# Optimization experiments

Measured on AMD Instinct MI355X. Metric: run time of the kernel, lower is better.

The kernel has to match this reference:

```python
import jax, jax.numpy as jnp
import numpy as np

B, S, D, H, C, E, V = 8, 2048, 1024, 512, 256, 64, 64


def setup_inputs() -> dict:
    key = jax.random.key(0)
    ks = jax.random.split(key, 40)
    ri = lambda i, hi: jax.random.randint(ks[i], (B, S), 0, hi).astype(jnp.int32)
    p = lambda i, shape: (jax.random.normal(ks[i], shape, jnp.float32) * 0.02)
    inp = {
        'h_x': jax.random.normal(ks[0], (B, S, D), jnp.float32),
        'h_y': jax.random.normal(ks[1], (B, S, D), jnp.float32),
        'x_mask': jnp.ones((B, S), jnp.int32),
        'y_mask': jnp.ones((B, S), jnp.int32),
        'src_token_dense_mask': ri(2, 2), 'src_token_sparse_mask': ri(3, 2),
        'src_token_inarc_type': ri(4, V), 'src_token_arc_head': ri(5, S),
        'src_token_depth': ri(6, 16), 'src_word_inarc_type': ri(7, V),
        'src_word_inarc_type_mask': ri(8, 2),
        'tgt_token_dense_mask': ri(9, 2), 'tgt_token_sparse_mask': ri(10, 2),
        'tgt_token_inarc_type': ri(11, V), 'tgt_token_arc_head': ri(12, S),
        'tgt_token_depth': ri(13, 16), 'tgt_word_inarc_type': ri(14, V),
        'tgt_word_inarc_type_mask': ri(15, 2),
        # src MLP [D->H->C], tgt MLP [D->H->C]
        'W1s': p(16, (D, H)), 'b1s': jnp.zeros((H,), jnp.float32),
        'W2s': p(17, (H, C)), 'b2s': jnp.zeros((C,), jnp.float32),
        'W1t': p(18, (D, H)), 'b1t': jnp.zeros((H,), jnp.float32),
        'W2t': p(19, (H, C)), 'b2t': jnp.zeros((C,), jnp.float32),
        # inarc edge embedding + GeneralConv params
        'emb': p(20, (V, E)),
        'W_msg': p(21, (C, C)), 'b_msg': jnp.zeros((C,), jnp.float32),
        'W_edge': p(22, (E, C)),
        'att': p(23, (C,)),
        'W_self': p(24, (C, C)), 'b_self': jnp.zeros((C,), jnp.float32),
        # axis_feature MLP [C->C]
        'Wf': p(25, (C, C)), 'bf': jnp.zeros((C,), jnp.float32),
    }
    return inp


def _mlp(h, W1, b1, W2, b2):
    return jax.nn.leaky_relu(h @ W1 + b1) @ W2 + b2


def _graph_side(h, dense_m, sparse_m, arc_head, word_type, word_mask,
                W1, b1, W2, b2, emb, W_msg, b_msg, W_edge, att, W_self, b_self, Wf, bf):
    Bn, Sn, _ = h.shape
    x = _mlp(h, W1, b1, W2, b2)                      # [B,S,C]
    N = Bn * Sn
    Cn = x.shape[-1]
    xg = x.reshape(N, Cn)                            # debatch -> nodes
    off = (jnp.arange(Bn, dtype=jnp.int32) * Sn)[:, None]
    src = (arc_head + off).reshape(N)                # global head index per token
    dst = jnp.arange(N, dtype=jnp.int32)             # one in-edge per token
    valid = (sparse_m * dense_m).reshape(N).astype(x.dtype)
    ef = emb[(word_type * word_mask).reshape(N)]     # [N,E] edge embeddings
    # GeneralConv: directed message with edge features + additive attention
    m = xg[src] @ W_msg + b_msg + ef @ W_edge        # [N,C] messages
    hd = xg @ W_msg + b_msg                          # dst-side term for attention
    logit = jax.nn.leaky_relu(((m + hd) * att).sum(-1))
    logit = jnp.where(valid > 0, logit, -1e9)
    emax = jax.ops.segment_max(logit, dst, num_segments=N)
    ex = jnp.exp(logit - emax[dst]) * valid
    den = jax.ops.segment_sum(ex, dst, num_segments=N)
    alpha = ex / (den[dst] + 1e-16)                  # softmax per destination node
    agg = jax.ops.segment_sum(m * alpha[:, None], dst, num_segments=N)
    out = xg @ W_self + b_self + agg                 # skip_linear
    out = out / jnp.maximum(jnp.linalg.norm(out, axis=-1, keepdims=True), 1e-12)
    r = out.reshape(Bn, Sn, Cn).mean(axis=1, keepdims=True)  # FeatureRepr mean
    return r @ Wf + bf                               # [B,1,C]


def reference(h_x, x_mask, src_token_dense_mask, src_token_sparse_mask,
              src_token_inarc_type, src_token_arc_head, src_token_depth,
              src_word_inarc_type, src_word_inarc_type_mask,
              h_y, y_mask, tgt_token_dense_mask, tgt_token_sparse_mask,
              tgt_token_inarc_type, tgt_token_arc_head, tgt_token_depth,
              tgt_word_inarc_type, tgt_word_inarc_type_mask,
              W1s, b1s, W2s, b2s, W1t, b1t, W2t, b2t,
              emb, W_msg, b_msg, W_edge, att, W_self, b_self, Wf, bf):
    src_repr = _graph_side(h_x, src_token_dense_mask, src_token_sparse_mask,
                           src_token_arc_head, src_word_inarc_type, src_word_inarc_type_mask,
                           W1s, b1s, W2s, b2s, emb, W_msg, b_msg, W_edge, att,
                           W_self, b_self, Wf, bf)
    tgt_repr = _graph_side(h_y, tgt_token_dense_mask, tgt_token_sparse_mask,
                           tgt_token_arc_head, tgt_word_inarc_type, tgt_word_inarc_type_mask,
                           W1t, b1t, W2t, b2t, emb, W_msg, b_msg, W_edge, att,
                           W_self, b_self, Wf, bf)
    return (src_repr, tgt_repr)
```

## Files before the change

kernel.cpp:

```cpp
#include <hip/hip_runtime.h>
#include <stdint.h>

#define SEQ   2048
#define NNODE 16384

typedef short  short8  __attribute__((ext_vector_type(8)));
typedef float  float4v __attribute__((ext_vector_type(4)));
typedef unsigned short u16;
typedef unsigned short u16x8 __attribute__((ext_vector_type(8)));
typedef short  short4v __attribute__((ext_vector_type(4)));

__device__ __forceinline__ float b2f(u16 u) {
    union { unsigned int i; float f; } x; x.i = ((unsigned int)u) << 16; return x.f;
}
__device__ __forceinline__ u16 f2b(float f) {
    union { float f; unsigned int i; } x; x.f = f;
    unsigned int u = x.i;
    unsigned int r = (u + 0x7fffu + ((u >> 16) & 1u)) >> 16;
    return (u16)r;
}

__device__ __forceinline__ void gld16(const void* g, void* l) {
    __builtin_amdgcn_global_load_lds(
        (const __attribute__((address_space(1))) void*)g,
        (__attribute__((address_space(3))) void*)l, 16, 0, 0);
}

__global__ __launch_bounds__(256) void cvt_k(const float* __restrict__ s0,
                                             const float* __restrict__ s1,
                                             u16* __restrict__ d) {
    const float* s = blockIdx.y ? s1 : s0;
    u16* dd = d + (size_t)blockIdx.y * 16777216u;
    const size_t i = ((size_t)blockIdx.x * 256 + threadIdx.x) * 8;
    float4v a = *(const float4v*)(s + i);
    float4v b = *(const float4v*)(s + i + 4);
    u16x8 r;
    r[0] = f2b(a[0]); r[1] = f2b(a[1]); r[2] = f2b(a[2]); r[3] = f2b(a[3]);
    r[4] = f2b(b[0]); r[5] = f2b(b[1]); r[6] = f2b(b[2]); r[7] = f2b(b[3]);
    *(u16x8*)(dd + i) = r;
}

struct GemmP {
    const u16*   A[4];
    const u16*   B[4];
    const float* bias[4];
    u16*         out[4];
};

template <int ACT>
__global__ __launch_bounds__(256) void gemm_k(GemmP p, int M, int N, int K) {
    __shared__ __align__(16) u16 As[128 * 64];
    __shared__ __align__(16) u16 Bs[128 * 64];

    const int z = blockIdx.z;
    const u16*   __restrict__ A    = p.A[z];
    const u16*   __restrict__ B    = p.B[z];
    const float* __restrict__ bias = p.bias[z];

    const int mt  = blockIdx.x * 128;
    const int nt  = blockIdx.y * 128;
    const int tid = threadIdx.x;
    const int l   = tid & 63;
    const int w   = tid >> 6;
    const int wm  = (w >> 1) * 64;
    const int wn  = (w & 1) * 64;
    const int lr  = l & 15;
    const int lk  = l >> 4;

    float4v acc[4][4] = {};

    for (int k0 = 0; k0 < K; k0 += 64) {
#pragma unroll
        for (int it = 0; it < 4; ++it) {
            int f  = it * 256 + tid;
            int rm = f >> 3, cc = f & 7;
            int gc = cc ^ (rm & 7);
            gld16(A + (size_t)(mt + rm) * K + (k0 + gc * 8), As + (size_t)f * 8);
            gld16(B + (size_t)(nt + rm) * K + (k0 + gc * 8), Bs + (size_t)f * 8);
        }
        __syncthreads();
#pragma unroll
        for (int ks = 0; ks < 2; ++ks) {
            short8 af[4], bfr[4];
            const int kc = ks * 4 + lk;
#pragma unroll
            for (int i = 0; i < 4; ++i) {
                int ra = wm + i * 16 + lr;
                af[i]  = *(const short8*)(As + ((size_t)ra * 8 + (kc ^ (ra & 7))) * 8);
                int rb = wn + i * 16 + lr;
                bfr[i] = *(const short8*)(Bs + ((size_t)rb * 8 + (kc ^ (rb & 7))) * 8);
            }
#pragma unroll
            for (int i = 0; i < 4; ++i)
#pragma unroll
                for (int j = 0; j < 4; ++j)
                    acc[i][j] = __builtin_amdgcn_mfma_f32_16x16x32_bf16(
                        af[i], bfr[j], acc[i][j], 0, 0, 0);
        }
        __syncthreads();
    }

    const int r0 = lk * 4;
#pragma unroll
    for (int j = 0; j < 4; ++j) {
        const int gn = nt + wn + j * 16 + lr;
        const float bv = bias[gn];
#pragma unroll
        for (int i = 0; i < 4; ++i) {
            const int gm = mt + wm + i * 16 + r0;
#pragma unroll
            for (int r = 0; r < 4; ++r) {
                float v = acc[i][j][r] + bv;
                if (ACT) v = v > 0.f ? v : 0.01f * v;
                p.out[z][(size_t)(gm + r) * N + gn] = f2b(v);
            }
        }
    }
}

struct TP { const float* src[6]; u16* dst[6]; int K[6]; int N[6]; };

__global__ void transpose_k(TP t) {
    const int m  = blockIdx.y;
    const int KN = t.K[m] * t.N[m];
    const int flat = blockIdx.x * 256 + threadIdx.x;
    if (flat >= KN) return;
    const int n = flat % t.N[m];
    const int k = flat / t.N[m];
    t.dst[m][(size_t)n * t.K[m] + k] = f2b(t.src[m][flat]);
}

__global__ void ew_k(const float* emb, const float* W_edge, float* EW) {
    const int t = blockIdx.x, c = threadIdx.x;
    float s = 0.f;
    for (int e = 0; e < 64; ++e)
        s += emb[t * 64 + e] * W_edge[e * 256 + c];
    EW[t * 256 + c] = s;
}

struct EpiP {
    const u16* xmsg[2]; const u16* xself[2];
    const int* den[2]; const int* spa[2]; const int* arc[2];
    const int* wty[2]; const int* wma[2];
    const float* EW; float* racc;
};

__global__ __launch_bounds__(256) void epi_k(EpiP p) {
    __shared__ float part[4][256];
    const int bx    = blockIdx.x;
    const int side  = bx >> 9;
    const int local = bx & 511;
    const int base  = local * 32;
    const int b     = base >> 11;
    const int tid   = threadIdx.x;
    const int w = tid >> 6, l = tid & 63;

    const u16* __restrict__ xmsg  = p.xmsg[side];
    const u16* __restrict__ xself = p.xself[side];

    float4v acc = {};
    for (int j = 0; j < 8; ++j) {
        const int i     = base + w * 8 + j;
        const int valid = p.den[side][i] * p.spa[side][i];
        const int srcn  = p.arc[side][i] + (i >> 11) * SEQ;
        const int t     = p.wty[side][i] * p.wma[side][i];
        short4v xs = *(const short4v*)(xself + (size_t)i * 256 + l * 4);
        short4v xm = *(const short4v*)(xmsg + (size_t)srcn * 256 + l * 4);
        float4v ew = *(const float4v*)(p.EW + (size_t)t * 256 + l * 4);
        const float vm = valid ? 1.f : 0.f;
        float4v v;
        v[0] = b2f((u16)xs[0]) + vm * (b2f((u16)xm[0]) + ew[0]);
        v[1] = b2f((u16)xs[1]) + vm * (b2f((u16)xm[1]) + ew[1]);
        v[2] = b2f((u16)xs[2]) + vm * (b2f((u16)xm[2]) + ew[2]);
        v[3] = b2f((u16)xs[3]) + vm * (b2f((u16)xm[3]) + ew[3]);
        float ss = v[0]*v[0] + v[1]*v[1] + v[2]*v[2] + v[3]*v[3];
        for (int m = 32; m >= 1; m >>= 1) ss += __shfl_xor(ss, m, 64);
        const float rn = 1.f / fmaxf(sqrtf(ss), 1e-12f);
        acc[0] += v[0] * rn; acc[1] += v[1] * rn;
        acc[2] += v[2] * rn; acc[3] += v[3] * rn;
    }
    part[w][l * 4 + 0] = acc[0];
    part[w][l * 4 + 1] = acc[1];
    part[w][l * 4 + 2] = acc[2];
    part[w][l * 4 + 3] = acc[3];
    __syncthreads();
    const float s = part[0][tid] + part[1][tid] + part[2][tid] + part[3][tid];
    atomicAdd(p.racc + ((size_t)side * 8 + b) * 256 + tid, s);
}

__global__ void fin_k(const float* racc, const float* Wf, const float* bfv,
                      float* out) {
    __shared__ float r[256];
    const int bid = blockIdx.x;
    const int tid = threadIdx.x;
    r[tid] = racc[bid * 256 + tid] * (1.f / 2048.f);
    __syncthreads();
    float s = bfv[tid];
    for (int k = 0; k < 256; ++k)
        s += r[k] * Wf[k * 256 + tid];
    out[bid * 256 + tid] = s;
}

extern "C" void kernel_launch(void* const* d_in, const int* in_sizes, int n_in,
                              void* d_out, int out_size, void* d_ws, size_t ws_size,
                              hipStream_t stream) {
    const float* h[2]   = {(const float*)d_in[0],  (const float*)d_in[1]};
    const int* den[2]   = {(const int*)d_in[4],  (const int*)d_in[11]};
    const int* spa[2]   = {(const int*)d_in[5],  (const int*)d_in[12]};
    const int* arc[2]   = {(const int*)d_in[7],  (const int*)d_in[14]};
    const int* wty[2]   = {(const int*)d_in[9],  (const int*)d_in[16]};
    const int* wma[2]   = {(const int*)d_in[10], (const int*)d_in[17]};
    const float* W1[2]  = {(const float*)d_in[18], (const float*)d_in[22]};
    const float* b1[2]  = {(const float*)d_in[19], (const float*)d_in[23]};
    const float* W2[2]  = {(const float*)d_in[20], (const float*)d_in[24]};
    const float* b2[2]  = {(const float*)d_in[21], (const float*)d_in[25]};
    const float* emb    = (const float*)d_in[26];
    const float* Wmsg   = (const float*)d_in[27];
    const float* bmsg   = (const float*)d_in[28];
    const float* Wedge  = (const float*)d_in[29];
    const float* Wself  = (const float*)d_in[31];
    const float* bself  = (const float*)d_in[32];
    const float* Wf     = (const float*)d_in[33];
    const float* bf_    = (const float*)d_in[34];

    char* ws = (char*)d_ws;
    size_t off = 0;
    auto alloc = [&](size_t bytes) -> void* {
        void* pp = ws + off; off += (bytes + 255) & ~(size_t)255; return pp;
    };
    u16*   hbf   = (u16*)  alloc(2ull * NNODE * 1024 * 2);
    u16*   x1    = (u16*)  alloc(2ull * NNODE * 512 * 2);
    u16*   xx    = (u16*)  alloc(2ull * NNODE * 256 * 2);
    u16*   W1T   = (u16*)  alloc(2ull * 512 * 1024 * 2);
    u16*   W2T   = (u16*)  alloc(2ull * 256 * 512 * 2);
    u16*   WmsgT = (u16*)  alloc(256 * 256 * 2);
    u16*   WselfT= (u16*)  alloc(256 * 256 * 2);
    float* EW    = (float*)alloc(64 * 256 * 4);
    float* racc  = (float*)alloc(2 * 8 * 256 * 4);
    u16*   xmsg  = hbf;
    u16*   xself = hbf + 2ull * NNODE * 256;

    hipLaunchKernelGGL(cvt_k, dim3(8192, 2), dim3(256), 0, stream,
                       h[0], h[1], hbf);
    TP tp;
    tp.src[0] = W1[0]; tp.dst[0] = W1T;              tp.K[0] = 1024; tp.N[0] = 512;
    tp.src[1] = W1[1]; tp.dst[1] = W1T + 512 * 1024; tp.K[1] = 1024; tp.N[1] = 512;
    tp.src[2] = W2[0]; tp.dst[2] = W2T;              tp.K[2] = 512;  tp.N[2] = 256;
    tp.src[3] = W2[1]; tp.dst[3] = W2T + 256 * 512;  tp.K[3] = 512;  tp.N[3] = 256;
    tp.src[4] = Wmsg;  tp.dst[4] = WmsgT;            tp.K[4] = 256;  tp.N[4] = 256;
    tp.src[5] = Wself; tp.dst[5] = WselfT;           tp.K[5] = 256;  tp.N[5] = 256;
    hipLaunchKernelGGL(transpose_k, dim3(2048, 6), dim3(256), 0, stream, tp);
    hipLaunchKernelGGL(ew_k, dim3(64), dim3(256), 0, stream, emb, Wedge, EW);
    hipMemsetAsync(racc, 0, 2 * 8 * 256 * 4, stream);

    GemmP g1 = {};
    g1.A[0] = hbf;   g1.A[1] = hbf + 2ull * NNODE * 512;
    g1.B[0] = W1T;   g1.B[1] = W1T + 512 * 1024;
    g1.bias[0] = b1[0]; g1.bias[1] = b1[1];
    g1.out[0] = x1;  g1.out[1] = x1 + (size_t)NNODE * 512;
    hipLaunchKernelGGL((gemm_k<1>), dim3(128, 4, 2), dim3(256), 0, stream,
                       g1, NNODE, 512, 1024);

    GemmP g2 = {};
    g2.A[0] = x1;  g2.A[1] = x1 + (size_t)NNODE * 512;
    g2.B[0] = W2T; g2.B[1] = W2T + 256 * 512;
    g2.bias[0] = b2[0]; g2.bias[1] = b2[1];
    g2.out[0] = xx; g2.out[1] = xx + (size_t)NNODE * 256;
    hipLaunchKernelGGL((gemm_k<0>), dim3(128, 2, 2), dim3(256), 0, stream,
                       g2, NNODE, 256, 512);

    GemmP g3 = {};
    g3.A[0] = xx; g3.A[1] = xx;
    g3.A[2] = xx + (size_t)NNODE * 256; g3.A[3] = xx + (size_t)NNODE * 256;
    g3.B[0] = WmsgT; g3.B[1] = WselfT; g3.B[2] = WmsgT; g3.B[3] = WselfT;
    g3.bias[0] = bmsg; g3.bias[1] = bself; g3.bias[2] = bmsg; g3.bias[3] = bself;
    g3.out[0] = xmsg;  g3.out[1] = xself;
    g3.out[2] = xmsg + (size_t)NNODE * 256; g3.out[3] = xself + (size_t)NNODE * 256;
    hipLaunchKernelGGL((gemm_k<0>), dim3(128, 2, 4), dim3(256), 0, stream,
                       g3, NNODE, 256, 256);

    EpiP ep;
    ep.xmsg[0]  = xmsg;  ep.xmsg[1]  = xmsg + (size_t)NNODE * 256;
    ep.xself[0] = xself; ep.xself[1] = xself + (size_t)NNODE * 256;
    for (int s = 0; s < 2; ++s) {
        ep.den[s] = den[s]; ep.spa[s] = spa[s]; ep.arc[s] = arc[s];
        ep.wty[s] = wty[s]; ep.wma[s] = wma[s];
    }
    ep.EW = EW; ep.racc = racc;
    hipLaunchKernelGGL(epi_k, dim3(1024), dim3(256), 0, stream, ep);

    hipLaunchKernelGGL(fin_k, dim3(16), dim3(256), 0, stream,
                       racc, Wf, bf_, (float*)d_out);
}
```

Before: 346.8 us.

## Fuse fp32-to-bf16 conversion into GEMM, stage epilogue via LDS, tile transposes

The separate kernel that converted the fp32 activations to bf16 is removed. The first GEMM now reads fp32 A directly, converts it in registers and stores it swizzled into LDS, which saves a full write and reread of the bf16 copy. The GEMM epilogue now stages its output tile in shared memory and writes coalesced 16-byte rows. The weight transpose uses 64x64 LDS tiles, and the msg/self projections are merged into one concatenated GEMM with a fused bias. The trade-off is that the first GEMM loses async global_load_lds for A and uses more LDS for the epilogue staging.

New measurement: 319.8 us. -7.8%, faster.

```diff
diff --git a/kernel.cpp b/kernel.cpp
--- a/kernel.cpp
+++ b/kernel.cpp
@@ -26,34 +26,22 @@
         (__attribute__((address_space(3))) void*)l, 16, 0, 0);
 }
 
-__global__ __launch_bounds__(256) void cvt_k(const float* __restrict__ s0,
-                                             const float* __restrict__ s1,
-                                             u16* __restrict__ d) {
-    const float* s = blockIdx.y ? s1 : s0;
-    u16* dd = d + (size_t)blockIdx.y * 16777216u;
-    const size_t i = ((size_t)blockIdx.x * 256 + threadIdx.x) * 8;
-    float4v a = *(const float4v*)(s + i);
-    float4v b = *(const float4v*)(s + i + 4);
-    u16x8 r;
-    r[0] = f2b(a[0]); r[1] = f2b(a[1]); r[2] = f2b(a[2]); r[3] = f2b(a[3]);
-    r[4] = f2b(b[0]); r[5] = f2b(b[1]); r[6] = f2b(b[2]); r[7] = f2b(b[3]);
-    *(u16x8*)(dd + i) = r;
-}
-
 struct GemmP {
-    const u16*   A[4];
-    const u16*   B[4];
-    const float* bias[4];
-    u16*         out[4];
+    const void*  A[2];
+    const u16*   B[2];
+    const float* bias[2];
+    u16*         out[2];
 };
 
-template <int ACT>
+#define LDW 136
+
+template <int ACT, int AF32>
 __global__ __launch_bounds__(256) void gemm_k(GemmP p, int M, int N, int K) {
-    __shared__ __align__(16) u16 As[128 * 64];
-    __shared__ __align__(16) u16 Bs[128 * 64];
+    __shared__ __align__(16) u16 smem[128 * LDW];
+    u16* As = smem;
+    u16* Bs = smem + 8192;
 
     const int z = blockIdx.z;
-    const u16*   __restrict__ A    = p.A[z];
     const u16*   __restrict__ B    = p.B[z];
     const float* __restrict__ bias = p.bias[z];
 
@@ -75,7 +63,20 @@
             int f  = it * 256 + tid;
             int rm = f >> 3, cc = f & 7;
             int gc = cc ^ (rm & 7);
-            gld16(A + (size_t)(mt + rm) * K + (k0 + gc * 8), As + (size_t)f * 8);
+            if (AF32) {
+                const float* __restrict__ A32 = (const float*)p.A[z];
+                const float* src = A32 + (size_t)(mt + rm) * K + (k0 + cc * 8);
+                float4v a = *(const float4v*)src;
+                float4v b = *(const float4v*)(src + 4);
+                u16x8 r;
+                r[0] = f2b(a[0]); r[1] = f2b(a[1]); r[2] = f2b(a[2]); r[3] = f2b(a[3]);
+                r[4] = f2b(b[0]); r[5] = f2b(b[1]); r[6] = f2b(b[2]); r[7] = f2b(b[3]);
+                *(u16x8*)(As + ((size_t)rm * 8 + (cc ^ (rm & 7))) * 8) = r;
+            } else {
+                const u16* __restrict__ A16 = (const u16*)p.A[z];
+                gld16(A16 + (size_t)(mt + rm) * K + (k0 + gc * 8),
+                      As + (size_t)f * 8);
+            }
             gld16(B + (size_t)(nt + rm) * K + (k0 + gc * 8), Bs + (size_t)f * 8);
         }
         __syncthreads();
@@ -103,31 +104,60 @@
     const int r0 = lk * 4;
 #pragma unroll
     for (int j = 0; j < 4; ++j) {
-        const int gn = nt + wn + j * 16 + lr;
-        const float bv = bias[gn];
+        const int lc = wn + j * 16 + lr;
+        const float bv = bias[nt + lc];
 #pragma unroll
         for (int i = 0; i < 4; ++i) {
-            const int gm = mt + wm + i * 16 + r0;
+            const int lrow = wm + i * 16 + r0;
 #pragma unroll
             for (int r = 0; r < 4; ++r) {
                 float v = acc[i][j][r] + bv;
                 if (ACT) v = v > 0.f ? v : 0.01f * v;
-                p.out[z][(size_t)(gm + r) * N + gn] = f2b(v);
+                smem[(size_t)(lrow + r) * LDW + lc] = f2b(v);
             }
         }
     }
+    __syncthreads();
+#pragma unroll
+    for (int pass = 0; pass < 8; ++pass) {
+        int id   = pass * 256 + tid;
+        int row  = id >> 4, colc = id & 15;
+        u16x8 vv = *(const u16x8*)(smem + (size_t)row * LDW + colc * 8);
+        *(u16x8*)(p.out[z] + (size_t)(mt + row) * N + nt + colc * 8) = vv;
+    }
 }
 
 struct TP { const float* src[6]; u16* dst[6]; int K[6]; int N[6]; };
 
-__global__ void transpose_k(TP t) {
-    const int m  = blockIdx.y;
-    const int KN = t.K[m] * t.N[m];
-    const int flat = blockIdx.x * 256 + threadIdx.x;
-    if (flat >= KN) return;
-    const int n = flat % t.N[m];
-    const int k = flat / t.N[m];
-    t.dst[m][(size_t)n * t.K[m] + k] = f2b(t.src[m][flat]);
+__global__ __launch_bounds__(256) void transpose_k(TP t) {
+    __shared__ float tile[64][65];
+    const int m = blockIdx.y;
+    const int K = t.K[m], N = t.N[m];
+    const int tn = N >> 6;
+    const int ntiles = (K >> 6) * tn;
+    const int bid = blockIdx.x;
+    if (bid >= ntiles) return;
+    const int k0 = (bid / tn) * 64, n0 = (bid % tn) * 64;
+    const int tid = threadIdx.x;
+#pragma unroll
+    for (int pass = 0; pass < 4; ++pass) {
+        int kk = pass * 16 + (tid >> 4);
+        int nn = (tid & 15) * 4;
+        float4v v = *(const float4v*)(t.src[m] + (size_t)(k0 + kk) * N + n0 + nn);
+        tile[kk][nn + 0] = v[0]; tile[kk][nn + 1] = v[1];
+        tile[kk][nn + 2] = v[2]; tile[kk][nn + 3] = v[3];
+    }
+    __syncthreads();
+    const int n = tid >> 2, kc = (tid & 3) * 16;
+    u16x8 a, b;
+#pragma unroll
+    for (int j = 0; j < 8; ++j) {
+        a[j] = f2b(tile[kc + j][n]);
+        b[j] = f2b(tile[kc + 8 + j][n]);
+    }
+    u16* d = t.dst[m] + (size_t)(n0 + n) * K + k0 + kc;
+    *(u16x8*)d = a;
+    *(u16x8*)(d + 8) = b;
 }
 
 __global__ void ew_k(const float* emb, const float* W_edge, float* EW) {
@@ -138,8 +168,14 @@
     EW[t * 256 + c] = s;
 }
 
+__global__ void bias_cat_k(const float* bmsg, const float* bself, float* bcat) {
+    const int tid = threadIdx.x;
+    bcat[tid]       = bmsg[tid];
+    bcat[256 + tid] = bself[tid];
+}
+
 struct EpiP {
-    const u16* xmsg[2]; const u16* xself[2];
+    const u16* xcat[2];
     const int* den[2]; const int* spa[2]; const int* arc[2];
     const int* wty[2]; const int* wma[2];
     const float* EW; float* racc;
@@ -155,8 +191,7 @@
     const int tid   = threadIdx.x;
     const int w = tid >> 6, l = tid & 63;
 
-    const u16* __restrict__ xmsg  = p.xmsg[side];
-    const u16* __restrict__ xself = p.xself[side];
+    const u16* __restrict__ xcat = p.xcat[side];
 
     float4v acc = {};
     for (int j = 0; j < 8; ++j) {
@@ -164,8 +199,8 @@
         const int valid = p.den[side][i] * p.spa[side][i];
         const int srcn  = p.arc[side][i] + (i >> 11) * SEQ;
         const int t     = p.wty[side][i] * p.wma[side][i];
-        short4v xs = *(const short4v*)(xself + (size_t)i * 256 + l * 4);
-        short4v xm = *(const short4v*)(xmsg + (size_t)srcn * 256 + l * 4);
+        short4v xs = *(const short4v*)(xcat + (size_t)i * 512 + 256 + l * 4);
+        short4v xm = *(const short4v*)(xcat + (size_t)srcn * 512 + l * 4);
         float4v ew = *(const float4v*)(p.EW + (size_t)t * 256 + l * 4);
         const float vm = valid ? 1.f : 0.f;
         float4v v;
@@ -228,37 +263,34 @@
     auto alloc = [&](size_t bytes) -> void* {
         void* pp = ws + off; off += (bytes + 255) & ~(size_t)255; return pp;
     };
-    u16*   hbf   = (u16*)  alloc(2ull * NNODE * 1024 * 2);
     u16*   x1    = (u16*)  alloc(2ull * NNODE * 512 * 2);
     u16*   xx    = (u16*)  alloc(2ull * NNODE * 256 * 2);
+    u16*   xcat  = (u16*)  alloc(2ull * NNODE * 512 * 2);
     u16*   W1T   = (u16*)  alloc(2ull * 512 * 1024 * 2);
     u16*   W2T   = (u16*)  alloc(2ull * 256 * 512 * 2);
-    u16*   WmsgT = (u16*)  alloc(256 * 256 * 2);
-    u16*   WselfT= (u16*)  alloc(256 * 256 * 2);
+    u16*   WcatT = (u16*)  alloc(512 * 256 * 2);
     float* EW    = (float*)alloc(64 * 256 * 4);
+    float* bcat  = (float*)alloc(512 * 4);
     float* racc  = (float*)alloc(2 * 8 * 256 * 4);
-    u16*   xmsg  = hbf;
-    u16*   xself = hbf + 2ull * NNODE * 256;
-
-    hipLaunchKernelGGL(cvt_k, dim3(8192, 2), dim3(256), 0, stream,
-                       h[0], h[1], hbf);
+
     TP tp;
     tp.src[0] = W1[0]; tp.dst[0] = W1T;              tp.K[0] = 1024; tp.N[0] = 512;
     tp.src[1] = W1[1]; tp.dst[1] = W1T + 512 * 1024; tp.K[1] = 1024; tp.N[1] = 512;
     tp.src[2] = W2[0]; tp.dst[2] = W2T;              tp.K[2] = 512;  tp.N[2] = 256;
     tp.src[3] = W2[1]; tp.dst[3] = W2T + 256 * 512;  tp.K[3] = 512;  tp.N[3] = 256;
-    tp.src[4] = Wmsg;  tp.dst[4] = WmsgT;            tp.K[4] = 256;  tp.N[4] = 256;
-    tp.src[5] = Wself; tp.dst[5] = WselfT;           tp.K[5] = 256;  tp.N[5] = 256;
-    hipLaunchKernelGGL(transpose_k, dim3(2048, 6), dim3(256), 0, stream, tp);
+    tp.src[4] = Wmsg;  tp.dst[4] = WcatT;            tp.K[4] = 256;  tp.N[4] = 256;
+    tp.src[5] = Wself; tp.dst[5] = WcatT + 256*256;  tp.K[5] = 256;  tp.N[5] = 256;
+    hipLaunchKernelGGL(transpose_k, dim3(128, 6), dim3(256), 0, stream, tp);
     hipLaunchKernelGGL(ew_k, dim3(64), dim3(256), 0, stream, emb, Wedge, EW);
+    hipLaunchKernelGGL(bias_cat_k, dim3(1), dim3(256), 0, stream, bmsg, bself, bcat);
     hipMemsetAsync(racc, 0, 2 * 8 * 256 * 4, stream);
 
     GemmP g1 = {};
-    g1.A[0] = hbf;   g1.A[1] = hbf + 2ull * NNODE * 512;
+    g1.A[0] = h[0];  g1.A[1] = h[1];
     g1.B[0] = W1T;   g1.B[1] = W1T + 512 * 1024;
     g1.bias[0] = b1[0]; g1.bias[1] = b1[1];
     g1.out[0] = x1;  g1.out[1] = x1 + (size_t)NNODE * 512;
-    hipLaunchKernelGGL((gemm_k<1>), dim3(128, 4, 2), dim3(256), 0, stream,
+    hipLaunchKernelGGL((gemm_k<1, 1>), dim3(128, 4, 2), dim3(256), 0, stream,
                        g1, NNODE, 512, 1024);
 
     GemmP g2 = {};
@@ -266,22 +298,19 @@
     g2.B[0] = W2T; g2.B[1] = W2T + 256 * 512;
     g2.bias[0] = b2[0]; g2.bias[1] = b2[1];
     g2.out[0] = xx; g2.out[1] = xx + (size_t)NNODE * 256;
-    hipLaunchKernelGGL((gemm_k<0>), dim3(128, 2, 2), dim3(256), 0, stream,
+    hipLaunchKernelGGL((gemm_k<0, 0>), dim3(128, 2, 2), dim3(256), 0, stream,
                        g2, NNODE, 256, 512);
 
     GemmP g3 = {};
-    g3.A[0] = xx; g3.A[1] = xx;
-    g3.A[2] = xx + (size_t)NNODE * 256; g3.A[3] = xx + (size_t)NNODE * 256;
-    g3.B[0] = WmsgT; g3.B[1] = WselfT; g3.B[2] = WmsgT; g3.B[3] = WselfT;
-    g3.bias[0] = bmsg; g3.bias[1] = bself; g3.bias[2] = bmsg; g3.bias[3] = bself;
-    g3.out[0] = xmsg;  g3.out[1] = xself;
-    g3.out[2] = xmsg + (size_t)NNODE * 256; g3.out[3] = xself + (size_t)NNODE * 256;
-    hipLaunchKernelGGL((gemm_k<0>), dim3(128, 2, 4), dim3(256), 0, stream,
-                       g3, NNODE, 256, 256);
+    g3.A[0] = xx;    g3.A[1] = xx + (size_t)NNODE * 256;
+    g3.B[0] = WcatT; g3.B[1] = WcatT;
+    g3.bias[0] = bcat; g3.bias[1] = bcat;
+    g3.out[0] = xcat;  g3.out[1] = xcat + (size_t)NNODE * 512;
+    hipLaunchKernelGGL((gemm_k<0, 0>), dim3(128, 4, 2), dim3(256), 0, stream,
+                       g3, NNODE, 512, 256);
 
     EpiP ep;
-    ep.xmsg[0]  = xmsg;  ep.xmsg[1]  = xmsg + (size_t)NNODE * 256;
-    ep.xself[0] = xself; ep.xself[1] = xself + (size_t)NNODE * 256;
+    ep.xcat[0] = xcat; ep.xcat[1] = xcat + (size_t)NNODE * 512;
     for (int s = 0; s < 2; ++s) {
         ep.den[s] = den[s]; ep.spa[s] = spa[s]; ep.arc[s] = arc[s];
         ep.wty[s] = wty[s]; ep.wma[s] = wma[s];
```
